# Kernel optimization log

Measured on AMD Instinct MI355X. Metric: run time of the kernel, lower is better.

Reference implementation:

```python
import jax, jax.numpy as jnp
import numpy as np

MARGIN = 1.0
B, D, NUM_CLASSES = 8192, 128, 10


def setup_inputs() -> dict:
    key = jax.random.key(0)
    k1, k2 = jax.random.split(key)
    embeddings = jax.random.normal(k1, (B, D), dtype=jnp.float32)
    labels = jax.random.randint(k2, (B,), 0, NUM_CLASSES, dtype=jnp.int64)
    return {"embeddings": embeddings, "labels": labels}


def reference(embeddings, labels):
    # pairwise Euclidean distances d[i, j] = sqrt(sum((e_i - e_j)^2))
    sq = jnp.sum(embeddings * embeddings, axis=-1)               # [B]
    d2 = sq[:, None] + sq[None, :] - 2.0 * (embeddings @ embeddings.T)
    dist = jnp.sqrt(jnp.maximum(d2, 0.0))                        # [B, B]

    same = labels[:, None] == labels[None, :]                    # [B, B] bool
    neg_inf = jnp.float32(-jnp.inf)
    pos_inf = jnp.float32(jnp.inf)

    # hardest positive: max distance among same-class (includes self, dist 0, harmless)
    hardest_pos = jnp.max(jnp.where(same, dist, neg_inf), axis=1)   # [B]
    # hardest negative: min distance among different-class
    hardest_neg = jnp.min(jnp.where(same, pos_inf, dist), axis=1)   # [B]

    per_anchor = jax.nn.relu(hardest_pos - hardest_neg + MARGIN)    # [B]
    # use_gt_than_zero_mean=False -> divide by batch size
    return jnp.sum(per_anchor) / per_anchor.shape[0]
```

## Files before the change

### kernel.cpp

```cpp
#include <hip/hip_runtime.h>
#include <hip/hip_bf16.h>
#include <cstdint>

#define BATCH 8192
#define DIM   128
#define KBYTES 192
#define MARGIN 1.0f
#define SEPI   193548
#define SCALE  16.0f
#define INVS2  (1.0f / 256.0f)

typedef __attribute__((ext_vector_type(4))) int   int4v;
typedef __attribute__((ext_vector_type(4))) float f32x4;

__device__ __forceinline__ void async_copy16(const void* g, void* lds) {
    __builtin_amdgcn_global_load_lds(
        (const __attribute__((address_space(1))) unsigned int*)g,
        (__attribute__((address_space(3))) unsigned int*)lds, 16, 0, 0);
}

__global__ __launch_bounds__(256) void bhtl_prep(
    const float* __restrict__ emb,
    const int* __restrict__ labels,
    signed char* __restrict__ EA,
    signed char* __restrict__ EB,
    int* __restrict__ sq,
    unsigned* __restrict__ hp2,
    unsigned* __restrict__ hn2)
{
    const int hw  = threadIdx.x >> 5;
    const int l   = threadIdx.x & 31;
    const int row = blockIdx.x * 8 + hw;
    const float4 e = ((const float4*)(emb + (size_t)row * DIM))[l];

    int a0 = (int)rintf(e.x * SCALE); a0 = min(127, max(-127, a0));
    int a1 = (int)rintf(e.y * SCALE); a1 = min(127, max(-127, a1));
    int a2 = (int)rintf(e.z * SCALE); a2 = min(127, max(-127, a2));
    int a3 = (int)rintf(e.w * SCALE); a3 = min(127, max(-127, a3));
    unsigned pa = (a0 & 255) | ((a1 & 255) << 8) | ((a2 & 255) << 16) | ((a3 & 255) << 24);
    *(unsigned*)(EA + (size_t)row * KBYTES + l * 4) = pa;
    *(unsigned*)(EB + (size_t)row * KBYTES + l * 4) = pa;

    if (l < 16) {
        const int lab = labels[row];
        unsigned wa = 0, wb = 0;
        #pragma unroll
        for (int b = 0; b < 4; ++b) {
            int j = l * 4 + b;
            int in = (j < 60) && (j / 6 == lab);
            wa |= (unsigned)((in ?  127 : 0) & 255) << (8 * b);
            wb |= (unsigned)((in ? -127 : 0) & 255) << (8 * b);
        }
        *(unsigned*)(EA + (size_t)row * KBYTES + 128 + l * 4) = wa;
        *(unsigned*)(EB + (size_t)row * KBYTES + 128 + l * 4) = wb;
    }

    int s = a0 * a0 + a1 * a1 + a2 * a2 + a3 * a3;
    #pragma unroll
    for (int d = 1; d < 32; d <<= 1) s += __shfl_xor(s, d, 64);
    if (l == 0) {
        sq[row]  = s;
        hp2[row] = 0u;
        hn2[row] = 0x7F800000u;
    }
}

__global__ __launch_bounds__(64) void bhtl_main(
    const signed char* __restrict__ EA,
    const signed char* __restrict__ EB,
    const int* __restrict__ sq,
    unsigned* __restrict__ hp2,
    unsigned* __restrict__ hn2)
{
    __shared__ __align__(16) unsigned char B_s[3][3072];
    __shared__ __align__(16) int sqm[512];

    const int lane = threadIdx.x;
    const int q    = lane >> 4;
    const int ln   = lane & 15;
    const int rb   = blockIdx.x >> 4;
    const int js   = blockIdx.x & 15;
    const int rowbase = rb * 64;
    const int jbase   = js * 512;

    int4v af[4][3];
    #pragma unroll
    for (int m = 0; m < 4; ++m)
        #pragma unroll
        for (int kc = 0; kc < 3; ++kc) {
            af[m][kc] = *(const int4v*)(
                EA + (size_t)(rowbase + m * 16 + ln) * KBYTES + kc * 64 + q * 16);
            asm("" : "+v"(af[m][kc]));
        }

    #pragma unroll
    for (int c = 0; c < 2; ++c)
        async_copy16(sq + jbase + (c * 64 + lane) * 4, &sqm[c * 256]);

    asm volatile("s_waitcnt vmcnt(0)" ::: "memory");

    const signed char* pB[3];
    #pragma unroll
    for (int c = 0; c < 3; ++c) {
        int U   = c * 64 + lane;
        int col = U / 12;
        int u   = U - col * 12;
        int g   = (u < 8) ? (u ^ (col & 7)) : (8 + ((u - 8) ^ (col & 3)));
        pB[c] = EB + (size_t)(jbase + col) * KBYTES + g * 16;
    }

    auto stageB = [&](int buf) {
        #pragma unroll
        for (int c = 0; c < 3; ++c) {
            async_copy16(pB[c], &B_s[buf][c * 1024]);
            pB[c] += 16 * KBYTES;
        }
    };

    int wmn[4] = {INT_MAX, INT_MAX, INT_MAX, INT_MAX};
    int wmx[4] = {INT_MIN, INT_MIN, INT_MIN, INT_MIN};

    auto doIter = [&](int ch, int buf, bool doStage, bool last) {
        if (last) asm volatile("s_waitcnt vmcnt(0)" ::: "memory");
        else      asm volatile("s_waitcnt vmcnt(3)" ::: "memory");

        int4v bfr[3];
        #pragma unroll
        for (int kc = 0; kc < 3; ++kc) {
            const int t    = kc * 4 + q;
            const int unit = (t < 8) ? (t ^ (ln & 7)) : (8 + (q ^ (ln & 3)));
            bfr[kc] = *(const int4v*)(&B_s[buf][(ln * 12 + unit) * 16]);
        }
        int4v sqj = *(const int4v*)(&sqm[ch * 16 + q * 4]);

        if (doStage) stageB((buf + 2) % 3);

        int4v acc[4];
        const int4v zero = {0, 0, 0, 0};
        #pragma unroll
        for (int m = 0; m < 4; ++m) acc[m] = zero;
        #pragma unroll
        for (int kc = 0; kc < 3; ++kc)
            #pragma unroll
            for (int m = 0; m < 4; ++m)
                acc[m] = __builtin_amdgcn_mfma_i32_16x16x64_i8(
                    bfr[kc], af[m][kc], acc[m], 0, 0, 0);

        const int nsq0 = -sqj[0], nsq1 = -sqj[1], nsq2 = -sqj[2], nsq3 = -sqj[3];
        #pragma unroll
        for (int m = 0; m < 4; ++m) {
            int w0 = acc[m][0] * 2 + nsq0;
            int w1 = acc[m][1] * 2 + nsq1;
            int w2 = acc[m][2] * 2 + nsq2;
            int w3 = acc[m][3] * 2 + nsq3;
            wmn[m] = min(wmn[m], min(min(w0, w1), min(w2, w3)));
            wmx[m] = max(wmx[m], max(max(w0, w1), max(w2, w3)));
        }
    };

    stageB(0);
    stageB(1);

    #pragma unroll 1
    for (int base = 0; base < 30; base += 3) {
        doIter(base,     0, true,           false);
        doIter(base + 1, 1, true,           false);
        doIter(base + 2, 2, base + 2 < 30,  false);
    }
    doIter(30, 0, false, false);
    doIter(31, 1, false, true);

    #pragma unroll
    for (int m = 0; m < 4; ++m) {
        int a = wmn[m], b = wmx[m];
        a = min(a, __shfl_xor(a, 16, 64));
        a = min(a, __shfl_xor(a, 32, 64));
        b = max(b, __shfl_xor(b, 16, 64));
        b = max(b, __shfl_xor(b, 32, 64));
        if (q == 0) {
            const int row = rowbase + m * 16 + ln;
            const int sqi = sq[row];
            float hpf = fmaxf((float)(sqi - a - SEPI) * INVS2, 0.0f);
            float hnf = fmaxf((float)(sqi - b) * INVS2, 0.0f);
            atomicMax(&hp2[row], __float_as_uint(hpf));
            atomicMin(&hn2[row], __float_as_uint(hnf));
        }
    }
}

__global__ __launch_bounds__(1024) void bhtl_final(
    const unsigned* __restrict__ hp2,
    const unsigned* __restrict__ hn2,
    float* __restrict__ out)
{
    __shared__ float red[16];
    float sum = 0.f;
    for (int i = threadIdx.x; i < BATCH; i += 1024) {
        float hp = sqrtf(__uint_as_float(hp2[i]));
        float hn = sqrtf(__uint_as_float(hn2[i]));
        sum += fmaxf(hp - hn + MARGIN, 0.f);
    }
    #pragma unroll
    for (int d = 1; d < 64; d <<= 1) sum += __shfl_xor(sum, d, 64);
    int wv = threadIdx.x >> 6;
    if ((threadIdx.x & 63) == 0) red[wv] = sum;
    __syncthreads();
    if (threadIdx.x < 64) {
        float v = (threadIdx.x < 16) ? red[threadIdx.x] : 0.f;
        #pragma unroll
        for (int d = 1; d < 16; d <<= 1) v += __shfl_xor(v, d, 64);
        if (threadIdx.x == 0) out[0] = v / (float)BATCH;
    }
}

extern "C" void kernel_launch(void* const* d_in, const int* in_sizes, int n_in,
                              void* d_out, int out_size, void* d_ws, size_t ws_size,
                              hipStream_t stream)
{
    const float* emb    = (const float*)d_in[0];
    const int*   labels = (const int*)d_in[1];
    float*       out    = (float*)d_out;

    char* ws = (char*)d_ws;
    signed char* EA  = (signed char*)ws;
    signed char* EB  = (signed char*)(ws + 2 * 1024 * 1024);
    int*      sq   = (int*)     (ws + 4 * 1024 * 1024);
    unsigned* hp2  = (unsigned*)(ws + 4 * 1024 * 1024 + 32 * 1024);
    unsigned* hn2  = (unsigned*)(ws + 4 * 1024 * 1024 + 64 * 1024);

    bhtl_prep<<<BATCH / 8, 256, 0, stream>>>(emb, labels, EA, EB, sq, hp2, hn2);
    bhtl_main<<<2048, 64, 0, stream>>>(EA, EB, sq, hp2, hn2);
    bhtl_final<<<1, 1024, 0, stream>>>(hp2, hn2, out);
}
```

Before: 80.82 us.

## Load B tiles directly into registers instead of staging through LDS

Replaces the async global-to-LDS triple-buffered staging of the B operand and squared norms with direct per-lane global loads into a three-slot register ring, prefetched two chunks ahead. It removes the LDS round trip, the swizzled LDS reads and the explicit waitcnt management. In exchange, each lane issues its own 16-byte global loads, which are less coalesced across rows of 192 bytes, raise register pressure and leave latency hiding to compiler-inserted waits.

```diff
diff --git a/kernel.cpp b/kernel.cpp
--- a/kernel.cpp
+++ b/kernel.cpp
@@ -12,12 +12,6 @@
 
 typedef __attribute__((ext_vector_type(4))) int   int4v;
 typedef __attribute__((ext_vector_type(4))) float f32x4;
-
-__device__ __forceinline__ void async_copy16(const void* g, void* lds) {
-    __builtin_amdgcn_global_load_lds(
-        (const __attribute__((address_space(1))) unsigned int*)g,
-        (__attribute__((address_space(3))) unsigned int*)lds, 16, 0, 0);
-}
 
 __global__ __launch_bounds__(256) void bhtl_prep(
     const float* __restrict__ emb,
@@ -72,9 +66,6 @@
     unsigned* __restrict__ hp2,
     unsigned* __restrict__ hn2)
 {
-    __shared__ __align__(16) unsigned char B_s[3][3072];
-    __shared__ __align__(16) int sqm[512];
-
     const int lane = threadIdx.x;
     const int q    = lane >> 4;
     const int ln   = lane & 15;
@@ -93,47 +84,28 @@
             asm("" : "+v"(af[m][kc]));
         }
 
-    #pragma unroll
-    for (int c = 0; c < 2; ++c)
-        async_copy16(sq + jbase + (c * 64 + lane) * 4, &sqm[c * 256]);
-
-    asm volatile("s_waitcnt vmcnt(0)" ::: "memory");
-
-    const signed char* pB[3];
-    #pragma unroll
-    for (int c = 0; c < 3; ++c) {
-        int U   = c * 64 + lane;
-        int col = U / 12;
-        int u   = U - col * 12;
-        int g   = (u < 8) ? (u ^ (col & 7)) : (8 + ((u - 8) ^ (col & 3)));
-        pB[c] = EB + (size_t)(jbase + col) * KBYTES + g * 16;
-    }
-
-    auto stageB = [&](int buf) {
-        #pragma unroll
-        for (int c = 0; c < 3; ++c) {
-            async_copy16(pB[c], &B_s[buf][c * 1024]);
-            pB[c] += 16 * KBYTES;
-        }
+    const signed char* pB  = EB + (size_t)(jbase + ln) * KBYTES + q * 16;
+    const int*         psq = sq + jbase + q * 4;
+
+    int4v bq[3][3];
+    int4v sv[3];
+
+    auto loadChunk = [&](int slot, int ch) {
+        const signed char* p = pB + (size_t)ch * (16 * KBYTES);
+        #pragma unroll
+        for (int kc = 0; kc < 3; ++kc)
+            bq[slot][kc] = *(const int4v*)(p + kc * 64);
+        sv[slot] = *(const int4v*)(psq + ch * 16);
     };
+
+    loadChunk(0, 0);
+    loadChunk(1, 1);
 
     int wmn[4] = {INT_MAX, INT_MAX, INT_MAX, INT_MAX};
     int wmx[4] = {INT_MIN, INT_MIN, INT_MIN, INT_MIN};
 
-    auto doIter = [&](int ch, int buf, bool doStage, bool last) {
-        if (last) asm volatile("s_waitcnt vmcnt(0)" ::: "memory");
-        else      asm volatile("s_waitcnt vmcnt(3)" ::: "memory");
-
-        int4v bfr[3];
-        #pragma unroll
-        for (int kc = 0; kc < 3; ++kc) {
-            const int t    = kc * 4 + q;
-            const int unit = (t < 8) ? (t ^ (ln & 7)) : (8 + (q ^ (ln & 3)));
-            bfr[kc] = *(const int4v*)(&B_s[buf][(ln * 12 + unit) * 16]);
-        }
-        int4v sqj = *(const int4v*)(&sqm[ch * 16 + q * 4]);
-
-        if (doStage) stageB((buf + 2) % 3);
+    auto doIter = [&](int ch, int slot, bool doPf, int pfSlot) {
+        if (doPf) loadChunk(pfSlot, ch + 2);
 
         int4v acc[4];
         const int4v zero = {0, 0, 0, 0};
@@ -144,8 +116,9 @@
             #pragma unroll
             for (int m = 0; m < 4; ++m)
                 acc[m] = __builtin_amdgcn_mfma_i32_16x16x64_i8(
-                    bfr[kc], af[m][kc], acc[m], 0, 0, 0);
-
+                    bq[slot][kc], af[m][kc], acc[m], 0, 0, 0);
+
+        const int4v sqj = sv[slot];
         const int nsq0 = -sqj[0], nsq1 = -sqj[1], nsq2 = -sqj[2], nsq3 = -sqj[3];
         #pragma unroll
         for (int m = 0; m < 4; ++m) {
@@ -158,17 +131,14 @@
         }
     };
 
-    stageB(0);
-    stageB(1);
-
     #pragma unroll 1
     for (int base = 0; base < 30; base += 3) {
-        doIter(base,     0, true,           false);
-        doIter(base + 1, 1, true,           false);
-        doIter(base + 2, 2, base + 2 < 30,  false);
-    }
-    doIter(30, 0, false, false);
-    doIter(31, 1, false, true);
+        doIter(base,     0, true,          2);
+        doIter(base + 1, 1, true,          0);
+        doIter(base + 2, 2, base + 2 < 30, 1);
+    }
+    doIter(30, 0, false, 0);
+    doIter(31, 1, false, 0);
 
     #pragma unroll
     for (int m = 0; m < 4; ++m) {
```

New measurement: 81.28 us. Within noise of the previous version (+0.6%).
